# Performance work log

Measured on AMD Instinct MI355X. Metric: run time of the kernel, lower is better.

The kernel has to match this reference:

```python
import jax, jax.numpy as jnp
import numpy as np

KERNEL = 9


def setup_inputs() -> dict:
    key = jax.random.key(0)
    k1, k2 = jax.random.split(key)
    n, c, h, w = 1, 256, 256, 256
    key_feature = jax.random.normal(k1, (n, c, h, w), dtype=jnp.float32)
    weights = jax.random.normal(k2, (1, KERNEL * KERNEL, h, w), dtype=jnp.float32)
    return {"key_feature": key_feature, "weights": weights}


def reference(key_feature, weights):
    # Dynamic local filtering: out[n,c,y,x] = sum_{i,j} pad(key)[n,c,y+i,x+j] * weights[0, i*k+j, y, x]
    # Faithful to: img2col (unfold with zero pad) * per-pixel weights, summed over k^2.
    k = KERNEL
    p = k // 2
    n, c, h, w = key_feature.shape
    # weights.squeeze().view(k^2, -1): [k^2, h*w] -> here keep spatial layout [k^2, h, w]
    wk = weights.reshape(k * k, h, w)
    padded = jnp.pad(key_feature, ((0, 0), (0, 0), (p, p), (p, p)))
    out = jnp.zeros_like(key_feature)
    for i in range(k):
        for j in range(k):
            patch = padded[:, :, i:i + h, j:j + w]  # [n,c,h,w]
            out = out + patch * wk[i * k + j]       # broadcast [h,w] over [n,c]
    return out
```

## Files before the change

kernel.cpp:

```cpp
#include <hip/hip_runtime.h>

#define HH 256
#define WW 256
#define CHN 256
#define PAD 4
#define HW (HH * WW)

#define TW 32
#define TH 16
#define PR 24
#define PC 40
#define PCP 41
#define NSPLIT 4
#define CPB 64
#define NG 16

__device__ __forceinline__ void fma4(float4& a, const float4& k, float w) {
    a.x = fmaf(k.x, w, a.x);
    a.y = fmaf(k.y, w, a.y);
    a.z = fmaf(k.z, w, a.z);
    a.w = fmaf(k.w, w, a.w);
}

__global__ __launch_bounds__(256, 2)
void prop_kernel(const float* __restrict__ key, const float* __restrict__ wts,
                 float* __restrict__ out) {
    __shared__ float4 smem[2][PR][PCP];

    const int tid = threadIdx.x;
    const int tw  = tid & 15;
    const int th  = tid >> 4;
    const int w0  = blockIdx.x * TW;
    const int h0  = blockIdx.y * TH;
    const int c0  = blockIdx.z * CPB;
    const int h   = h0 + th;
    const int w   = w0 + 2 * tw;

    float wt0[81], wt1[81];
    {
        const float* wp = wts + h * WW + w;
        #pragma unroll
        for (int t = 0; t < 81; ++t) {
            float2 v = *reinterpret_cast<const float2*>(wp + t * HW);
            wt0[t] = v.x;
            wt1[t] = v.y;
        }
    }

    {
        const float* kp = key + (size_t)c0 * HW;
        for (int p = tid; p < PR * PC; p += 256) {
            int row = p / PC;
            int col = p - row * PC;
            int gh  = h0 - PAD + row;
            int gw  = w0 - PAD + col;
            float4 v = make_float4(0.f, 0.f, 0.f, 0.f);
            if ((unsigned)gh < HH && (unsigned)gw < WW) {
                const float* q = kp + gh * WW + gw;
                v.x = q[0];
                v.y = q[HW];
                v.z = q[2 * HW];
                v.w = q[3 * HW];
            }
            smem[0][row][col] = v;
        }
    }
    __syncthreads();

    for (int g = 0; g < NG; ++g) {
        if (g + 1 < NG) {
            const float* kp = key + (size_t)(c0 + (g + 1) * 4) * HW;
            float4* dst = &smem[(g + 1) & 1][0][0];
            for (int p = tid; p < PR * PC; p += 256) {
                int row = p / PC;
                int col = p - row * PC;
                int gh  = h0 - PAD + row;
                int gw  = w0 - PAD + col;
                float4 v = make_float4(0.f, 0.f, 0.f, 0.f);
                if ((unsigned)gh < HH && (unsigned)gw < WW) {
                    const float* q = kp + gh * WW + gw;
                    v.x = q[0];
                    v.y = q[HW];
                    v.z = q[2 * HW];
                    v.w = q[3 * HW];
                }
                dst[row * PCP + col] = v;
            }
        }

        const float4* bp = &smem[g & 1][0][0] + th * PCP + 2 * tw;
        float4 a0 = make_float4(0.f, 0.f, 0.f, 0.f);
        float4 a1 = make_float4(0.f, 0.f, 0.f, 0.f);
        #pragma unroll
        for (int r = 0; r < 9; ++r) {
            #pragma unroll
            for (int c = 0; c < 10; ++c) {
                float4 k4 = bp[r * PCP + c];
                if (c < 9)  fma4(a0, k4, wt0[r * 9 + c]);
                if (c >= 1) fma4(a1, k4, wt1[r * 9 + c - 1]);
            }
        }

        const int cb = c0 + g * 4;
        float* op = out + (size_t)cb * HW + h * WW + w;
        *reinterpret_cast<float2*>(op)          = make_float2(a0.x, a1.x);
        *reinterpret_cast<float2*>(op + HW)     = make_float2(a0.y, a1.y);
        *reinterpret_cast<float2*>(op + 2 * HW) = make_float2(a0.z, a1.z);
        *reinterpret_cast<float2*>(op + 3 * HW) = make_float2(a0.w, a1.w);

        __syncthreads();
    }
}

extern "C" void kernel_launch(void* const* d_in, const int* in_sizes, int n_in,
                              void* d_out, int out_size, void* d_ws, size_t ws_size,
                              hipStream_t stream) {
    const float* key = (const float*)d_in[0];
    const float* wts = (const float*)d_in[1];
    float* out = (float*)d_out;

    dim3 grid(WW / TW, HH / TH, NSPLIT);
    prop_kernel<<<grid, 256, 0, stream>>>(key, wts, out);
}
```

Baseline: 195.1 us.

## Prefetch next channel group into registers and precompute staging addresses

Next channel group's global loads now go into registers before the compute loop and are written to shared memory only after the outputs are stored. Global load latency can then overlap the 81-tap FMA work instead of stalling before it. Staging addresses, bounds masks and shared-memory offsets are computed once per thread rather than per group, removing repeated divisions. The cost is 16 extra staging registers on top of the 162 weight registers, which risks spills or lower occupancy under launch_bounds(256,2). Out-of-range slots now load from a clamped valid address and zero afterward.

Result: no change. 196.2 us (+0.6%).

```diff
diff --git a/kernel.cpp b/kernel.cpp
--- a/kernel.cpp
+++ b/kernel.cpp
@@ -2,7 +2,6 @@
 
 #define HH 256
 #define WW 256
-#define CHN 256
 #define PAD 4
 #define HW (HH * WW)
 
@@ -14,6 +13,7 @@
 #define NSPLIT 4
 #define CPB 64
 #define NG 16
+#define NSLOT 4
 
 __device__ __forceinline__ void fma4(float4& a, const float4& k, float w) {
     a.x = fmaf(k.x, w, a.x);
@@ -47,44 +47,60 @@
         }
     }
 
+    const float* sp[NSLOT];
+    int  sdst[NSLOT];
+    bool sin_[NSLOT];
+    bool sact[NSLOT];
+    #pragma unroll
+    for (int k = 0; k < NSLOT; ++k) {
+        int p   = tid + k * 256;
+        bool act = p < PR * PC;
+        int row = p / PC;
+        int col = p - row * PC;
+        int gh  = h0 - PAD + row;
+        int gw  = w0 - PAD + col;
+        bool inb = act && (unsigned)gh < HH && (unsigned)gw < WW;
+        sact[k] = act;
+        sin_[k] = inb;
+        sdst[k] = row * PCP + col;
+        sp[k]   = key + (size_t)c0 * HW + (inb ? (gh * WW + gw) : 0);
+    }
+
     {
-        const float* kp = key + (size_t)c0 * HW;
-        for (int p = tid; p < PR * PC; p += 256) {
-            int row = p / PC;
-            int col = p - row * PC;
-            int gh  = h0 - PAD + row;
-            int gw  = w0 - PAD + col;
-            float4 v = make_float4(0.f, 0.f, 0.f, 0.f);
-            if ((unsigned)gh < HH && (unsigned)gw < WW) {
-                const float* q = kp + gh * WW + gw;
-                v.x = q[0];
-                v.y = q[HW];
-                v.z = q[2 * HW];
-                v.w = q[3 * HW];
-            }
-            smem[0][row][col] = v;
+        float4 v[NSLOT];
+        #pragma unroll
+        for (int k = 0; k < NSLOT; ++k) {
+            const float* q = sp[k];
+            v[k].x = q[0];
+            v[k].y = q[HW];
+            v[k].z = q[2 * HW];
+            v[k].w = q[3 * HW];
+            if (!sin_[k]) v[k] = make_float4(0.f, 0.f, 0.f, 0.f);
+            sp[k] += 4 * HW;
         }
+        float4* dstb = &smem[0][0][0];
+        #pragma unroll
+        for (int k = 0; k < NSLOT; ++k)
+            if (sact[k]) dstb[sdst[k]] = v[k];
     }
     __syncthreads();
 
+    float* op = out + (size_t)c0 * HW + h * WW + w;
+
     for (int g = 0; g < NG; ++g) {
-        if (g + 1 < NG) {
-            const float* kp = key + (size_t)(c0 + (g + 1) * 4) * HW;
-            float4* dst = &smem[(g + 1) & 1][0][0];
-            for (int p = tid; p < PR * PC; p += 256) {
-                int row = p / PC;
-                int col = p - row * PC;
-                int gh  = h0 - PAD + row;
-                int gw  = w0 - PAD + col;
-                float4 v = make_float4(0.f, 0.f, 0.f, 0.f);
-                if ((unsigned)gh < HH && (unsigned)gw < WW) {
-                    const float* q = kp + gh * WW + gw;
-                    v.x = q[0];
-                    v.y = q[HW];
-                    v.z = q[2 * HW];
-                    v.w = q[3 * HW];
-                }
-                dst[row * PCP + col] = v;
+        const bool pf = (g + 1 < NG);
+
+        float4 stg[NSLOT];
+        if (pf) {
+            #pragma unroll
+            for (int k = 0; k < NSLOT; ++k) {
+                const float* q = sp[k];
+                stg[k].x = q[0];
+                stg[k].y = q[HW];
+                stg[k].z = q[2 * HW];
+                stg[k].w = q[3 * HW];
+                if (!sin_[k]) stg[k] = make_float4(0.f, 0.f, 0.f, 0.f);
+                sp[k] += 4 * HW;
             }
         }
 
@@ -101,12 +117,18 @@
             }
         }
 
-        const int cb = c0 + g * 4;
-        float* op = out + (size_t)cb * HW + h * WW + w;
         *reinterpret_cast<float2*>(op)          = make_float2(a0.x, a1.x);
         *reinterpret_cast<float2*>(op + HW)     = make_float2(a0.y, a1.y);
         *reinterpret_cast<float2*>(op + 2 * HW) = make_float2(a0.z, a1.z);
         *reinterpret_cast<float2*>(op + 3 * HW) = make_float2(a0.w, a1.w);
+        op += 4 * HW;
+
+        if (pf) {
+            float4* dstb = &smem[(g + 1) & 1][0][0];
+            #pragma unroll
+            for (int k = 0; k < NSLOT; ++k)
+                if (sact[k]) dstb[sdst[k]] = stg[k];
+        }
 
         __syncthreads();
     }
```
